# Kernel tuning notes

Measured on AMD Instinct MI355X. Metric: run time of the kernel, lower is better.

## Reference

```python
import jax, jax.numpy as jnp
import numpy as np

LAMBDA_GEO = 0.5


def setup_inputs() -> dict:
    key = jax.random.key(0)
    embeddings = jax.random.normal(key, (4, 2048, 512), dtype=jnp.float32)
    return {"embeddings": embeddings}


def _geometric_loss(embeddings):
    b, s, d = embeddings.shape
    x = embeddings.reshape(b * s, d)  # [N, d]
    sq_norm = jnp.sum(x * x, axis=-1)  # [N]
    sq = sq_norm[:, None] + sq_norm[None, :] - 2.0 * (x @ x.T)  # [N, N]
    sq = jnp.maximum(sq, 0.0)
    dist = jnp.sqrt(sq)  # torch.cdist(p=2)
    return jnp.mean(jnp.exp(-dist * 0.1)) * 0.1


def reference(embeddings):
    geometric_loss = _geometric_loss(embeddings)
    total_geometric = LAMBDA_GEO * geometric_loss
    return geometric_loss, total_geometric
```

## Files before the change

### kernel.cpp

```cpp
#include <hip/hip_runtime.h>

#define NROWS 8192
#define DIM   512
#define NT    64
#define NTRI  (NT * (NT + 1) / 2)
#define NACC  64

using bf16x8 = __attribute__((ext_vector_type(8))) __bf16;
using f32x4  = __attribute__((ext_vector_type(4))) float;

__device__ __forceinline__ ushort f2bf(float f) {
    unsigned u = __float_as_uint(f);
    unsigned r = u + 0x7fffu + ((u >> 16) & 1u);
    return (ushort)(r >> 16);
}

__global__ __launch_bounds__(256) void norm_convert_kernel(
    const float* __restrict__ X, ushort* __restrict__ Xb,
    float* __restrict__ norms, float* __restrict__ acc)
{
    const int tid  = threadIdx.x;
    const int lane = tid & 63;
    const int w    = tid >> 6;
    const int row  = blockIdx.x * 4 + w;

    if (blockIdx.x == 0 && tid < NACC) acc[tid] = 0.0f;

    const float* xr = X + (size_t)row * DIM + lane * 8;
    float4 v0 = *(const float4*)xr;
    float4 v1 = *(const float4*)(xr + 4);

    float s = 0.0f;
    s = fmaf(v0.x, v0.x, s); s = fmaf(v0.y, v0.y, s);
    s = fmaf(v0.z, v0.z, s); s = fmaf(v0.w, v0.w, s);
    s = fmaf(v1.x, v1.x, s); s = fmaf(v1.y, v1.y, s);
    s = fmaf(v1.z, v1.z, s); s = fmaf(v1.w, v1.w, s);

    union { ushort u16[8]; uint4 v; } pk;
    pk.u16[0] = f2bf(v0.x); pk.u16[1] = f2bf(v0.y);
    pk.u16[2] = f2bf(v0.z); pk.u16[3] = f2bf(v0.w);
    pk.u16[4] = f2bf(v1.x); pk.u16[5] = f2bf(v1.y);
    pk.u16[6] = f2bf(v1.z); pk.u16[7] = f2bf(v1.w);
    *(uint4*)(Xb + (size_t)row * DIM + lane * 8) = pk.v;

    #pragma unroll
    for (int off = 32; off > 0; off >>= 1) s += __shfl_down(s, off, 64);
    if (lane == 0) norms[row] = s;
}

__global__ __launch_bounds__(256, 4) void pair_loss_gemm_kernel(
    const ushort* __restrict__ Xb, const float* __restrict__ norms,
    float* __restrict__ acc)
{
    __shared__ __align__(16) ushort As0[128 * 32];
    __shared__ __align__(16) ushort As1[128 * 32];
    __shared__ __align__(16) ushort Bs0[128 * 32];
    __shared__ __align__(16) ushort Bs1[128 * 32];
    __shared__ float wsum[4];

    int t = blockIdx.x, bi = 0;
    while (t >= (NT - bi)) { t -= (NT - bi); bi++; }
    const int bj = bi + t;

    const int tid  = threadIdx.x;
    const int lane = tid & 63;
    const int w    = tid >> 6;

    const int rowA = bi * 128;
    const int rowB = bj * 128;

    f32x4 accv[4][4];
    const f32x4 zero = {0.0f, 0.0f, 0.0f, 0.0f};
    #pragma unroll
    for (int a = 0; a < 4; a++)
        #pragma unroll
        for (int b = 0; b < 4; b++) accv[a][b] = zero;

    const int r0  = tid >> 2;
    const int o0  = (tid & 3) * 8;
    const int lws = r0 * 32 + o0;
    const ushort* gA0 = Xb + (size_t)(rowA + r0) * DIM + o0;
    const ushort* gA1 = gA0 + (size_t)64 * DIM;
    const ushort* gB0 = Xb + (size_t)(rowB + r0) * DIM + o0;
    const ushort* gB1 = gB0 + (size_t)64 * DIM;

    const int fr = lane & 15;
    const int kq = (lane >> 4) * 8;
    const int wr = (w & 1) * 64;
    const int wc = (w >> 1) * 64;

    {
        uint4 pa0 = *(const uint4*)gA0;
        uint4 pa1 = *(const uint4*)gA1;
        uint4 pb0 = *(const uint4*)gB0;
        uint4 pb1 = *(const uint4*)gB1;
        *(uint4*)(As0 + lws)        = pa0;
        *(uint4*)(As0 + lws + 2048) = pa1;
        *(uint4*)(Bs0 + lws)        = pb0;
        *(uint4*)(Bs0 + lws + 2048) = pb1;
    }
    __syncthreads();

    ushort* curA = As0; ushort* nxtA = As1;
    ushort* curB = Bs0; ushort* nxtB = Bs1;

    #pragma unroll 1
    for (int k = 0; k < 16; k++) {
        uint4 pa0, pa1, pb0, pb1;
        const bool more = (k < 15);
        if (more) {
            const int k0 = (k + 1) * 32;
            pa0 = *(const uint4*)(gA0 + k0);
            pa1 = *(const uint4*)(gA1 + k0);
            pb0 = *(const uint4*)(gB0 + k0);
            pb1 = *(const uint4*)(gB1 + k0);
        }

        bf16x8 af[4], bfr[4];
        #pragma unroll
        for (int a = 0; a < 4; a++)
            af[a] = *(const bf16x8*)(curA + (wr + a * 16 + fr) * 32 + kq);
        #pragma unroll
        for (int b = 0; b < 4; b++)
            bfr[b] = *(const bf16x8*)(curB + (wc + b * 16 + fr) * 32 + kq);

        #pragma unroll
        for (int a = 0; a < 4; a++)
            #pragma unroll
            for (int b = 0; b < 4; b++)
                accv[a][b] = __builtin_amdgcn_mfma_f32_16x16x32_bf16(
                    af[a], bfr[b], accv[a][b], 0, 0, 0);

        if (more) {
            *(uint4*)(nxtA + lws)        = pa0;
            *(uint4*)(nxtA + lws + 2048) = pa1;
            *(uint4*)(nxtB + lws)        = pb0;
            *(uint4*)(nxtB + lws + 2048) = pb1;
            __syncthreads();
            ushort* tA = curA; curA = nxtA; nxtA = tA;
            ushort* tB = curB; curB = nxtB; nxtB = tB;
        }
    }

    const float wgt = (bi == bj) ? 1.0f : 2.0f;
    float lsum = 0.0f;
    #pragma unroll
    for (int a = 0; a < 4; a++) {
        const int gi0 = rowA + wr + a * 16 + (lane >> 4) * 4;
        #pragma unroll
        for (int b = 0; b < 4; b++) {
            const int gj = rowB + wc + b * 16 + (lane & 15);
            const float nj = norms[gj];
            #pragma unroll
            for (int r = 0; r < 4; r++) {
                const int gi = gi0 + r;
                float sq = fmaf(-2.0f, accv[a][b][r], norms[gi] + nj);
                sq = fmaxf(sq, 0.0f);
                float term = __expf(-0.1f * sqrtf(sq));
                if (gi == gj) term = 1.0f;
                lsum += term;
            }
        }
    }
    lsum *= wgt;
    #pragma unroll
    for (int off = 32; off > 0; off >>= 1) lsum += __shfl_down(lsum, off, 64);
    if (lane == 0) wsum[w] = lsum;
    __syncthreads();
    if (tid == 0)
        atomicAdd(&acc[blockIdx.x & (NACC - 1)],
                  wsum[0] + wsum[1] + wsum[2] + wsum[3]);
}

__global__ void finalize_kernel(const float* __restrict__ acc,
                                float* __restrict__ out)
{
    const int lane = threadIdx.x;
    float s = (lane < NACC) ? acc[lane] : 0.0f;
    #pragma unroll
    for (int off = 32; off > 0; off >>= 1) s += __shfl_down(s, off, 64);
    if (lane == 0) {
        const float inv = 1.0f / ((float)NROWS * (float)NROWS);
        float loss = s * inv * 0.1f;
        out[0] = loss;
        out[1] = 0.5f * loss;
    }
}

extern "C" void kernel_launch(void* const* d_in, const int* in_sizes, int n_in,
                              void* d_out, int out_size, void* d_ws, size_t ws_size,
                              hipStream_t stream)
{
    const float* X = (const float*)d_in[0];
    float* out = (float*)d_out;

    char* ws = (char*)d_ws;
    float*  acc   = (float*)ws;
    float*  norms = (float*)(ws + 1024);
    ushort* Xb    = (ushort*)(ws + 1024 + 32768);

    norm_convert_kernel<<<NROWS / 4, 256, 0, stream>>>(X, Xb, norms, acc);
    pair_loss_gemm_kernel<<<NTRI, 256, 0, stream>>>(Xb, norms, acc);
    finalize_kernel<<<1, 64, 0, stream>>>(acc, out);
}
```

Baseline: 120.0 us.

## Swizzle LDS tile layout and fold finalize into GEMM via last-block counter

XORs the 8-element column chunk index with row bits when storing and reading the bf16 tiles in shared memory, so MFMA fragment reads are spread across LDS banks. It also removes the separate finalize kernel: each block bumps an atomic counter after adding its partial sum, and the last block reduces the accumulators and writes both outputs. This saves one kernel launch and cuts LDS bank conflicts, at the cost of an extra fence and atomic per block.

```diff
diff --git a/kernel.cpp b/kernel.cpp
--- a/kernel.cpp
+++ b/kernel.cpp
@@ -17,14 +17,18 @@
 
 __global__ __launch_bounds__(256) void norm_convert_kernel(
     const float* __restrict__ X, ushort* __restrict__ Xb,
-    float* __restrict__ norms, float* __restrict__ acc)
+    float* __restrict__ norms, float* __restrict__ acc,
+    unsigned* __restrict__ counter)
 {
     const int tid  = threadIdx.x;
     const int lane = tid & 63;
     const int w    = tid >> 6;
     const int row  = blockIdx.x * 4 + w;
 
-    if (blockIdx.x == 0 && tid < NACC) acc[tid] = 0.0f;
+    if (blockIdx.x == 0) {
+        if (tid < NACC) acc[tid] = 0.0f;
+        if (tid == NACC) *counter = 0u;
+    }
 
     const float* xr = X + (size_t)row * DIM + lane * 8;
     float4 v0 = *(const float4*)xr;
@@ -50,13 +54,15 @@
 
 __global__ __launch_bounds__(256, 4) void pair_loss_gemm_kernel(
     const ushort* __restrict__ Xb, const float* __restrict__ norms,
-    float* __restrict__ acc)
+    float* __restrict__ acc, unsigned* __restrict__ counter,
+    float* __restrict__ out)
 {
     __shared__ __align__(16) ushort As0[128 * 32];
     __shared__ __align__(16) ushort As1[128 * 32];
     __shared__ __align__(16) ushort Bs0[128 * 32];
     __shared__ __align__(16) ushort Bs1[128 * 32];
     __shared__ float wsum[4];
+    __shared__ int   is_last;
 
     int t = blockIdx.x, bi = 0;
     while (t >= (NT - bi)) { t -= (NT - bi); bi++; }
@@ -77,15 +83,17 @@
         for (int b = 0; b < 4; b++) accv[a][b] = zero;
 
     const int r0  = tid >> 2;
-    const int o0  = (tid & 3) * 8;
-    const int lws = r0 * 32 + o0;
-    const ushort* gA0 = Xb + (size_t)(rowA + r0) * DIM + o0;
+    const int c0  = tid & 3;
+    const int cs  = c0 ^ ((r0 >> 1) & 3);
+    const int lws = r0 * 32 + cs * 8;
+    const ushort* gA0 = Xb + (size_t)(rowA + r0) * DIM + c0 * 8;
     const ushort* gA1 = gA0 + (size_t)64 * DIM;
-    const ushort* gB0 = Xb + (size_t)(rowB + r0) * DIM + o0;
+    const ushort* gB0 = Xb + (size_t)(rowB + r0) * DIM + c0 * 8;
     const ushort* gB1 = gB0 + (size_t)64 * DIM;
 
     const int fr = lane & 15;
-    const int kq = (lane >> 4) * 8;
+    const int cc = (lane >> 4) ^ ((fr >> 1) & 3);
+    const int fo = fr * 32 + cc * 8;
     const int wr = (w & 1) * 64;
     const int wc = (w >> 1) * 64;
 
@@ -119,10 +127,10 @@
         bf16x8 af[4], bfr[4];
         #pragma unroll
         for (int a = 0; a < 4; a++)
-            af[a] = *(const bf16x8*)(curA + (wr + a * 16 + fr) * 32 + kq);
+            af[a] = *(const bf16x8*)(curA + (wr + a * 16) * 32 + fo);
         #pragma unroll
         for (int b = 0; b < 4; b++)
-            bfr[b] = *(const bf16x8*)(curB + (wc + b * 16 + fr) * 32 + kq);
+            bfr[b] = *(const bf16x8*)(curB + (wc + b * 16) * 32 + fo);
 
         #pragma unroll
         for (int a = 0; a < 4; a++)
@@ -167,23 +175,28 @@
     for (int off = 32; off > 0; off >>= 1) lsum += __shfl_down(lsum, off, 64);
     if (lane == 0) wsum[w] = lsum;
     __syncthreads();
-    if (tid == 0)
+
+    if (tid == 0) {
         atomicAdd(&acc[blockIdx.x & (NACC - 1)],
                   wsum[0] + wsum[1] + wsum[2] + wsum[3]);
-}
-
-__global__ void finalize_kernel(const float* __restrict__ acc,
-                                float* __restrict__ out)
-{
-    const int lane = threadIdx.x;
-    float s = (lane < NACC) ? acc[lane] : 0.0f;
-    #pragma unroll
-    for (int off = 32; off > 0; off >>= 1) s += __shfl_down(s, off, 64);
-    if (lane == 0) {
-        const float inv = 1.0f / ((float)NROWS * (float)NROWS);
-        float loss = s * inv * 0.1f;
-        out[0] = loss;
-        out[1] = 0.5f * loss;
+        __threadfence();
+        unsigned prev = atomicAdd(counter, 1u);
+        is_last = (prev == NTRI - 1) ? 1 : 0;
+    }
+    __syncthreads();
+    if (is_last) {
+        __threadfence();
+        if (tid < 64) {
+            float s = acc[tid];
+            #pragma unroll
+            for (int off = 32; off > 0; off >>= 1) s += __shfl_down(s, off, 64);
+            if (tid == 0) {
+                const float inv = 1.0f / ((float)NROWS * (float)NROWS);
+                float loss = s * inv * 0.1f;
+                out[0] = loss;
+                out[1] = 0.5f * loss;
+            }
+        }
     }
 }
 
@@ -195,11 +208,11 @@
     float* out = (float*)d_out;
 
     char* ws = (char*)d_ws;
-    float*  acc   = (float*)ws;
-    float*  norms = (float*)(ws + 1024);
-    ushort* Xb    = (ushort*)(ws + 1024 + 32768);
-
-    norm_convert_kernel<<<NROWS / 4, 256, 0, stream>>>(X, Xb, norms, acc);
-    pair_loss_gemm_kernel<<<NTRI, 256, 0, stream>>>(Xb, norms, acc);
-    finalize_kernel<<<1, 64, 0, stream>>>(acc, out);
-}
+    float*    acc     = (float*)ws;
+    unsigned* counter = (unsigned*)(ws + 512);
+    float*    norms   = (float*)(ws + 1024);
+    ushort*   Xb      = (ushort*)(ws + 1024 + 32768);
+
+    norm_convert_kernel<<<NROWS / 4, 256, 0, stream>>>(X, Xb, norms, acc, counter);
+    pair_loss_gemm_kernel<<<NTRI, 256, 0, stream>>>(Xb, norms, acc, counter, out);
+}
```

After: 156.3 us. +30.2%, slower.

## Swizzle LDS tile layout and deepen global prefetch with unrolled double buffer

Applied to the files above, without the earlier changes.

Applies an XOR swizzle to the 16-byte chunk index in the shared-memory tiles, so that MFMA fragment reads from different rows land in different LDS banks. The k-loop is unrolled by two with fixed buffers and two register sets (P and Q), so global loads are issued two stages ahead instead of one. This is meant to cut LDS bank conflicts and hide more global-memory latency. In exchange it uses more registers, which could reduce occupancy under the launch bound of four blocks.

```diff
diff --git a/kernel.cpp b/kernel.cpp
--- a/kernel.cpp
+++ b/kernel.cpp
@@ -77,68 +77,87 @@
         for (int b = 0; b < 4; b++) accv[a][b] = zero;
 
     const int r0  = tid >> 2;
-    const int o0  = (tid & 3) * 8;
-    const int lws = r0 * 32 + o0;
-    const ushort* gA0 = Xb + (size_t)(rowA + r0) * DIM + o0;
+    const int c0  = tid & 3;
+    const int cs  = c0 ^ ((r0 >> 1) & 3);
+    const int lws = r0 * 32 + cs * 8;
+    const ushort* gA0 = Xb + (size_t)(rowA + r0) * DIM + c0 * 8;
     const ushort* gA1 = gA0 + (size_t)64 * DIM;
-    const ushort* gB0 = Xb + (size_t)(rowB + r0) * DIM + o0;
+    const ushort* gB0 = Xb + (size_t)(rowB + r0) * DIM + c0 * 8;
     const ushort* gB1 = gB0 + (size_t)64 * DIM;
 
     const int fr = lane & 15;
-    const int kq = (lane >> 4) * 8;
+    const int cc = (lane >> 4) ^ ((fr >> 1) & 3);
+    const int fo = fr * 32 + cc * 8;
     const int wr = (w & 1) * 64;
     const int wc = (w >> 1) * 64;
 
-    {
-        uint4 pa0 = *(const uint4*)gA0;
-        uint4 pa1 = *(const uint4*)gA1;
-        uint4 pb0 = *(const uint4*)gB0;
-        uint4 pb1 = *(const uint4*)gB1;
-        *(uint4*)(As0 + lws)        = pa0;
-        *(uint4*)(As0 + lws + 2048) = pa1;
-        *(uint4*)(Bs0 + lws)        = pb0;
-        *(uint4*)(Bs0 + lws + 2048) = pb1;
-    }
+    uint4 Pa0, Pa1, Pb0, Pb1;
+    uint4 Qa0, Qa1, Qb0, Qb1;
+
+    Pa0 = *(const uint4*)gA0;  Pa1 = *(const uint4*)gA1;
+    Pb0 = *(const uint4*)gB0;  Pb1 = *(const uint4*)gB1;
+    *(uint4*)(As0 + lws)        = Pa0;
+    *(uint4*)(As0 + lws + 2048) = Pa1;
+    *(uint4*)(Bs0 + lws)        = Pb0;
+    *(uint4*)(Bs0 + lws + 2048) = Pb1;
+    Pa0 = *(const uint4*)(gA0 + 32);  Pa1 = *(const uint4*)(gA1 + 32);
+    Pb0 = *(const uint4*)(gB0 + 32);  Pb1 = *(const uint4*)(gB1 + 32);
     __syncthreads();
 
-    ushort* curA = As0; ushort* nxtA = As1;
-    ushort* curB = Bs0; ushort* nxtB = Bs1;
-
     #pragma unroll 1
-    for (int k = 0; k < 16; k++) {
-        uint4 pa0, pa1, pb0, pb1;
-        const bool more = (k < 15);
-        if (more) {
-            const int k0 = (k + 1) * 32;
-            pa0 = *(const uint4*)(gA0 + k0);
-            pa1 = *(const uint4*)(gA1 + k0);
-            pb0 = *(const uint4*)(gB0 + k0);
-            pb1 = *(const uint4*)(gB1 + k0);
-        }
-
-        bf16x8 af[4], bfr[4];
-        #pragma unroll
-        for (int a = 0; a < 4; a++)
-            af[a] = *(const bf16x8*)(curA + (wr + a * 16 + fr) * 32 + kq);
-        #pragma unroll
-        for (int b = 0; b < 4; b++)
-            bfr[b] = *(const bf16x8*)(curB + (wc + b * 16 + fr) * 32 + kq);
-
-        #pragma unroll
-        for (int a = 0; a < 4; a++)
+    for (int k = 0; k < 16; k += 2) {
+        if (k + 2 < 16) {
+            const int k0 = (k + 2) * 32;
+            Qa0 = *(const uint4*)(gA0 + k0);  Qa1 = *(const uint4*)(gA1 + k0);
+            Qb0 = *(const uint4*)(gB0 + k0);  Qb1 = *(const uint4*)(gB1 + k0);
+        }
+        {
+            bf16x8 af[4], bfr[4];
+            #pragma unroll
+            for (int a = 0; a < 4; a++)
+                af[a] = *(const bf16x8*)(As0 + (wr + a * 16) * 32 + fo);
             #pragma unroll
             for (int b = 0; b < 4; b++)
-                accv[a][b] = __builtin_amdgcn_mfma_f32_16x16x32_bf16(
-                    af[a], bfr[b], accv[a][b], 0, 0, 0);
-
-        if (more) {
-            *(uint4*)(nxtA + lws)        = pa0;
-            *(uint4*)(nxtA + lws + 2048) = pa1;
-            *(uint4*)(nxtB + lws)        = pb0;
-            *(uint4*)(nxtB + lws + 2048) = pb1;
+                bfr[b] = *(const bf16x8*)(Bs0 + (wc + b * 16) * 32 + fo);
+            #pragma unroll
+            for (int a = 0; a < 4; a++)
+                #pragma unroll
+                for (int b = 0; b < 4; b++)
+                    accv[a][b] = __builtin_amdgcn_mfma_f32_16x16x32_bf16(
+                        af[a], bfr[b], accv[a][b], 0, 0, 0);
+        }
+        *(uint4*)(As1 + lws)        = Pa0;
+        *(uint4*)(As1 + lws + 2048) = Pa1;
+        *(uint4*)(Bs1 + lws)        = Pb0;
+        *(uint4*)(Bs1 + lws + 2048) = Pb1;
+        __syncthreads();
+
+        if (k + 3 < 16) {
+            const int k0 = (k + 3) * 32;
+            Pa0 = *(const uint4*)(gA0 + k0);  Pa1 = *(const uint4*)(gA1 + k0);
+            Pb0 = *(const uint4*)(gB0 + k0);  Pb1 = *(const uint4*)(gB1 + k0);
+        }
+        {
+            bf16x8 af[4], bfr[4];
+            #pragma unroll
+            for (int a = 0; a < 4; a++)
+                af[a] = *(const bf16x8*)(As1 + (wr + a * 16) * 32 + fo);
+            #pragma unroll
+            for (int b = 0; b < 4; b++)
+                bfr[b] = *(const bf16x8*)(Bs1 + (wc + b * 16) * 32 + fo);
+            #pragma unroll
+            for (int a = 0; a < 4; a++)
+                #pragma unroll
+                for (int b = 0; b < 4; b++)
+                    accv[a][b] = __builtin_amdgcn_mfma_f32_16x16x32_bf16(
+                        af[a], bfr[b], accv[a][b], 0, 0, 0);
+        }
+        if (k + 2 < 16) {
+            *(uint4*)(As0 + lws)        = Qa0;
+            *(uint4*)(As0 + lws + 2048) = Qa1;
+            *(uint4*)(Bs0 + lws)        = Qb0;
+            *(uint4*)(Bs0 + lws + 2048) = Qb1;
             __syncthreads();
-            ushort* tA = curA; curA = nxtA; nxtA = tA;
-            ushort* tB = curB; curB = nxtB; nxtB = tB;
         }
     }
 
```

After: 154.8 us. 1.29x slower.
